# Kernel tuning notes

Measured on AMD Instinct MI355X. Metric: run time of the kernel, lower is better.

The kernel has to match this reference:

```python
import jax, jax.numpy as jnp
import numpy as np

N_NODES = 50000


def _gcn_layer(x, src, dst, W, b, n_nodes):
    # PyG GCNConv: h = x @ W, add self-loops, sym-normalized scatter-add, + bias
    h = x @ W  # [N, Dout]
    loop = jnp.arange(n_nodes, dtype=src.dtype)
    src2 = jnp.concatenate([src, loop])
    dst2 = jnp.concatenate([dst, loop])
    ones = jnp.ones(src2.shape[0], dtype=x.dtype)
    deg = jax.ops.segment_sum(ones, dst2, num_segments=n_nodes)  # in-degree w/ self-loops
    dinv = jnp.where(deg > 0, jax.lax.rsqrt(deg), 0.0)
    norm = dinv[src2] * dinv[dst2]  # [E+N]
    msg = h[src2] * norm[:, None]   # gather + scale
    out = jax.ops.segment_sum(msg, dst2, num_segments=n_nodes)  # scatter-add
    return out + b


def setup_inputs() -> dict:
    key = jax.random.key(0)
    k1, k2, k3, k4 = jax.random.split(key, 4)
    x = jax.random.normal(k1, (N_NODES, 128), dtype=jnp.float32)
    edge_index = jax.random.randint(k2, (2, 500000), 0, N_NODES, dtype=jnp.int64)
    W1 = jax.random.normal(k3, (128, 128), dtype=jnp.float32) * (1.0 / np.sqrt(128))
    b1 = jnp.zeros((128,), dtype=jnp.float32)
    W2 = jax.random.normal(k4, (128, 64), dtype=jnp.float32) * (1.0 / np.sqrt(128))
    b2 = jnp.zeros((64,), dtype=jnp.float32)
    return {"x": x, "edge_index": edge_index, "W1": W1, "b1": b1, "W2": W2, "b2": b2}


def reference(x, edge_index, W1, b1, W2, b2):
    src, dst = edge_index[0], edge_index[1]
    n = x.shape[0]
    h = _gcn_layer(x, src, dst, W1, b1, n)
    h = jax.nn.relu(h)
    out = _gcn_layer(h, src, dst, W2, b2, n)
    return out
```

## Files before the change

kernel.cpp:

```cpp
#include <hip/hip_runtime.h>
#include <hip/hip_bf16.h>
#include <cstddef>


typedef __attribute__((ext_vector_type(8))) short short8;
typedef __attribute__((ext_vector_type(4))) float f32x4;
typedef unsigned long long u64;

__device__ inline unsigned short f2bf(float f) {
    __hip_bfloat16 b = __float2bfloat16(f);
    return *reinterpret_cast<unsigned short*>(&b);
}
__device__ inline float bf2f_lo(unsigned int u) {
    unsigned int v = u << 16;
    return *reinterpret_cast<float*>(&v);
}
__device__ inline float bf2f_hi(unsigned int u) {
    unsigned int v = u & 0xffff0000u;
    return *reinterpret_cast<float*>(&v);
}
__device__ inline u64 ld_acq64(u64* p) {
    return __hip_atomic_load(p, __ATOMIC_ACQUIRE, __HIP_MEMORY_SCOPE_AGENT);
}
__device__ inline void st_rel64(u64* p, u64 v) {
    __hip_atomic_store(p, v, __ATOMIC_RELEASE, __HIP_MEMORY_SCOPE_AGENT);
}

__global__ __launch_bounds__(256) void init_kernel(int* __restrict__ deg, int N,
                                                   const float* __restrict__ W1,
                                                   const float* __restrict__ W2,
                                                   unsigned short* __restrict__ W1f,
                                                   unsigned short* __restrict__ W2f,
                                                   u64* __restrict__ lb, int ZB) {
    int b = blockIdx.x;
    int tid = threadIdx.x;
    if (b < ZB) {
        int i = (b * 256 + tid) * 4;
        if (i + 3 < N) *(int4*)(deg + i) = make_int4(0, 0, 0, 0);
        else for (; i < N; i++) deg[i] = 0;
        return;
    }
    int idx = (b - ZB) * 256 + tid;
    if (idx < 64) lb[idx] = 0;
    if (idx < 3072) {
        const float* W;
        unsigned short* Wf;
        int n, oct, Nc;
        if (idx < 2048) { W = W1; Wf = W1f; Nc = 128; n = idx >> 4; oct = idx & 15; }
        else { W = W2; Wf = W2f; Nc = 64; int i2 = idx - 2048; n = i2 >> 4; oct = i2 & 15; }
        int k0 = oct * 8;
        int ks = k0 >> 5, quad = (k0 >> 3) & 3, ntg = n >> 4;
        short8 v;
        #pragma unroll
        for (int j = 0; j < 8; j++) v[j] = (short)f2bf(W[(k0 + j) * Nc + n]);
        int off = (((ntg * 4 + ks) * 64) + (n & 15) + 16 * quad) * 8;
        *(short8*)(Wf + off) = v;
    }
}

__global__ __launch_bounds__(256) void countgemm_kernel(
    const int* __restrict__ dst, int E,
    int* __restrict__ deg, unsigned short* __restrict__ rank,
    const unsigned short* __restrict__ W1f,
    const float* __restrict__ x, unsigned short* __restrict__ h1,
    int N, int CB) {

    int b = blockIdx.x;
    int tid = threadIdx.x;

    __shared__ unsigned short As[64 * 128];

    if (b < CB) {
        int i = (b * 256 + tid) * 4;
        if (i + 3 < E) {
            int4 d = *(const int4*)(dst + i);
            unsigned short r0 = (unsigned short)atomicAdd(&deg[d.x], 1);
            unsigned short r1 = (unsigned short)atomicAdd(&deg[d.y], 1);
            unsigned short r2 = (unsigned short)atomicAdd(&deg[d.z], 1);
            unsigned short r3 = (unsigned short)atomicAdd(&deg[d.w], 1);
            *(ushort4*)(rank + i) = make_ushort4(r0, r1, r2, r3);
        } else {
            for (; i < E; i++) rank[i] = (unsigned short)atomicAdd(&deg[dst[i]], 1);
        }
        return;
    }

    constexpr int K = 128, BN = 128;
    int lane = tid & 63;
    int w = tid >> 6;
    int row0 = (b - CB) * 64;

    short8 bfr[2][4];
    #pragma unroll
    for (int nl = 0; nl < 2; nl++)
        #pragma unroll
        for (int ks = 0; ks < 4; ks++)
            bfr[nl][ks] = *(const short8*)(W1f + ((((w * 2 + nl) * 4 + ks) * 64) + lane) * 8);

    #pragma unroll
    for (int it = 0; it < 8; it++) {
        int idx = it * 256 + tid;
        int row = idx >> 5, kq = idx & 31;
        int k0 = kq * 4;
        int ks = k0 >> 5, quad = (k0 >> 3) & 3, j0 = k0 & 7, mt = row >> 4;
        ushort4 o = make_ushort4(0, 0, 0, 0);
        int gr = row0 + row;
        if (gr < N) {
            float4 a = *(const float4*)(x + (size_t)gr * K + k0);
            o.x = f2bf(a.x); o.y = f2bf(a.y); o.z = f2bf(a.z); o.w = f2bf(a.w);
        }
        int off = (((mt * 4 + ks) * 64) + (row & 15) + 16 * quad) * 8 + j0;
        *(ushort4*)(As + off) = o;
    }
    __syncthreads();

    f32x4 acc[4][2];
    #pragma unroll
    for (int mt = 0; mt < 4; mt++)
        #pragma unroll
        for (int nl = 0; nl < 2; nl++) acc[mt][nl] = (f32x4){0.f, 0.f, 0.f, 0.f};

    #pragma unroll
    for (int ks = 0; ks < 4; ks++) {
        short8 af[4];
        #pragma unroll
        for (int mt = 0; mt < 4; mt++)
            af[mt] = *(const short8*)(As + (((mt * 4 + ks) * 64) + lane) * 8);
        #pragma unroll
        for (int mt = 0; mt < 4; mt++)
            #pragma unroll
            for (int nl = 0; nl < 2; nl++)
                acc[mt][nl] = __builtin_amdgcn_mfma_f32_16x16x32_bf16(
                    af[mt], bfr[nl][ks], acc[mt][nl], 0, 0, 0);
    }

    int col16 = lane & 15;
    int rowq = lane >> 4;
    #pragma unroll
    for (int mt = 0; mt < 4; mt++) {
        #pragma unroll
        for (int nl = 0; nl < 2; nl++) {
            int gc = (w * 2 + nl) * 16 + col16;
            #pragma unroll
            for (int r = 0; r < 4; r++) {
                int lr = mt * 16 + rowq * 4 + r;
                int gr = row0 + lr;
                if (gr < N) h1[(size_t)gr * BN + gc] = f2bf(acc[mt][nl][r]);
            }
        }
    }
}

__global__ __launch_bounds__(256) void scan_lb_kernel(const int* __restrict__ deg, int N,
                                                      u64* __restrict__ lb,
                                                      int* __restrict__ offs,
                                                      float* __restrict__ dinv) {
    __shared__ int ws[4];
    __shared__ int s_prefix;
    int tid = threadIdx.x;
    int sb = blockIdx.x;
    int SB = gridDim.x;
    int lane = tid & 63;
    int wv = tid >> 6;

    int i = sb * 1024 + tid * 4;
    int v0 = (i + 0 < N) ? deg[i + 0] : 0;
    int v1 = (i + 1 < N) ? deg[i + 1] : 0;
    int v2 = (i + 2 < N) ? deg[i + 2] : 0;
    int v3 = (i + 3 < N) ? deg[i + 3] : 0;
    int tsum = v0 + v1 + v2 + v3;
    int xs = tsum;
    #pragma unroll
    for (int off = 1; off < 64; off <<= 1) {
        int y = __shfl_up(xs, off, 64);
        if (lane >= off) xs += y;
    }
    if (lane == 63) ws[wv] = xs;
    __syncthreads();
    int wprefix = 0;
    #pragma unroll
    for (int w2 = 0; w2 < 4; w2++) wprefix += (w2 < wv) ? ws[w2] : 0;
    int chunk_total = ws[0] + ws[1] + ws[2] + ws[3];

    if (wv == 0) {
        if (lane == 0)
            st_rel64(&lb[sb], ((u64)(unsigned)chunk_total << 2) | 1ull);
        int contrib = 0;
        if (sb > 0) {
            int pred = sb - 1 - lane;
            for (;;) {
                u64 v = (pred >= 0) ? ld_acq64(&lb[pred]) : 2ull;
                int flag = (int)(v & 3);
                u64 ball2 = __ballot(flag == 2);
                u64 ball0 = __ballot(flag == 0);
                if (ball2 != 0) {
                    int L = __ffsll(ball2) - 1;
                    if ((ball0 & ((1ull << L) - 1)) == 0) {
                        contrib = (lane <= L) ? (int)(unsigned)(v >> 2) : 0;
                        break;
                    }
                }
                __builtin_amdgcn_s_sleep(1);
            }
            #pragma unroll
            for (int off = 32; off >= 1; off >>= 1)
                contrib += __shfl_xor(contrib, off, 64);
        }
        if (lane == 0) {
            st_rel64(&lb[sb], ((u64)(unsigned)(contrib + chunk_total) << 2) | 2ull);
            s_prefix = contrib;
        }
    }
    __syncthreads();

    int carry = s_prefix;
    int e0 = carry + wprefix + xs - tsum;
    int e1 = e0 + v0, e2 = e1 + v1, e3 = e2 + v2;
    if (i + 0 < N) { offs[i + 0] = e0; dinv[i + 0] = rsqrtf((float)(v0 + 1)); }
    if (i + 1 < N) { offs[i + 1] = e1; dinv[i + 1] = rsqrtf((float)(v1 + 1)); }
    if (i + 2 < N) { offs[i + 2] = e2; dinv[i + 2] = rsqrtf((float)(v2 + 1)); }
    if (i + 3 < N) { offs[i + 3] = e3; dinv[i + 3] = rsqrtf((float)(v3 + 1)); }
    if (sb == SB - 1 && tid == 0) offs[N] = carry + chunk_total;
}

__global__ __launch_bounds__(256) void fill_kernel(
    const int* __restrict__ src, const int* __restrict__ dst, int E,
    const int* __restrict__ offs, const unsigned short* __restrict__ rank,
    int* __restrict__ csr) {
    int i = (blockIdx.x * 256 + threadIdx.x) * 4;
    if (i + 3 < E) {
        int4 s4 = *(const int4*)(src + i);
        int4 d4 = *(const int4*)(dst + i);
        ushort4 r4 = *(const ushort4*)(rank + i);
        csr[offs[d4.x] + (int)r4.x] = s4.x;
        csr[offs[d4.y] + (int)r4.y] = s4.y;
        csr[offs[d4.z] + (int)r4.z] = s4.z;
        csr[offs[d4.w] + (int)r4.w] = s4.w;
    } else {
        for (; i < E; i++) csr[offs[dst[i]] + (int)rank[i]] = src[i];
    }
}

__global__ __launch_bounds__(256) void aggmm_kernel(const unsigned short* __restrict__ h1,
                                                    const int* __restrict__ offs,
                                                    const int* __restrict__ csr,
                                                    const float* __restrict__ dinv,
                                                    const float* __restrict__ b1,
                                                    const unsigned short* __restrict__ W2f,
                                                    unsigned short* __restrict__ h2,
                                                    int n) {
    __shared__ unsigned short As[4 * 64 * 8];

    int tid = threadIdx.x;
    int t = tid & 63;
    int w = tid >> 6;
    int p = t >> 5;
    int t5 = t & 31;
    int nodebase = blockIdx.x * 16;
    int node0 = nodebase + w * 4;

    int ov = offs[min(node0 + min(t, 4), n)];
    int e0a[4], dega[4], nba[4], cidx[4];
    float cdw[4], dia[4];
    #pragma unroll
    for (int i = 0; i < 4; i++) {
        e0a[i] = __shfl(ov, i, 64);
        dega[i] = __shfl(ov, i + 1, 64) - e0a[i];
        nba[i] = min(dega[i], 64);
        int ce = e0a[i] + min(t, max(dega[i] - 1, 0));
        bool has = dega[i] > 0;
        cidx[i] = has ? csr[ce] : 0;
        cdw[i] = has ? dinv[cidx[i]] : 0.f;
        int node = node0 + i;
        dia[i] = (node < n) ? dinv[node] : 0.f;
    }

    short8 bw[4];
    #pragma unroll
    for (int ks = 0; ks < 4; ks++)
        bw[ks] = *(const short8*)(W2f + (((w * 4 + ks) * 64) + t) * 8);

    float4 bias = *(const float4*)(b1 + t5 * 4);

    #pragma unroll
    for (int i = 0; i < 4; i++) {
        int row16 = w * 4 + i;
        int node = node0 + i;
        float a0 = 0.f, a1 = 0.f, a2 = 0.f, a3 = 0.f;
        if (node < n) {
            if (p == 0) {
                uint2 su = *(const uint2*)(h1 + (size_t)node * 128 + t5 * 4);
                a0 = bf2f_lo(su.x) * dia[i]; a1 = bf2f_hi(su.x) * dia[i];
                a2 = bf2f_lo(su.y) * dia[i]; a3 = bf2f_hi(su.y) * dia[i];
            }
            for (int jb = 0; jb < nba[i]; jb += 8) {
                #pragma unroll
                for (int j = 0; j < 4; j++) {
                    int ee = jb + j * 2 + p;
                    int ec = min(ee, nba[i] - 1);
                    int s = __shfl(cidx[i], ec, 64);
                    float wraw = __shfl(cdw[i], ec, 64);
                    float wgt = (ee < nba[i]) ? wraw : 0.f;
                    uint2 hu = *(const uint2*)(h1 + (size_t)s * 128 + t5 * 4);
                    a0 += bf2f_lo(hu.x) * wgt; a1 += bf2f_hi(hu.x) * wgt;
                    a2 += bf2f_lo(hu.y) * wgt; a3 += bf2f_hi(hu.y) * wgt;
                }
            }
            int e1 = e0a[i] + dega[i];
            for (int eb = e0a[i] + 64; eb < e1; eb += 8) {
                #pragma unroll
                for (int j = 0; j < 4; j++) {
                    int ee = eb + j * 2 + p;
                    int ec = min(ee, e1 - 1);
                    int s = csr[ec];
                    float wgt = (ee < e1) ? dinv[s] : 0.f;
                    uint2 hu = *(const uint2*)(h1 + (size_t)s * 128 + t5 * 4);
                    a0 += bf2f_lo(hu.x) * wgt; a1 += bf2f_hi(hu.x) * wgt;
                    a2 += bf2f_lo(hu.y) * wgt; a3 += bf2f_hi(hu.y) * wgt;
                }
            }
        }
        a0 += __shfl_xor(a0, 32, 64);
        a1 += __shfl_xor(a1, 32, 64);
        a2 += __shfl_xor(a2, 32, 64);
        a3 += __shfl_xor(a3, 32, 64);
        if (p == 0) {
            if (node < n) {
                a0 = fmaxf(a0 * dia[i] + bias.x, 0.f);
                a1 = fmaxf(a1 * dia[i] + bias.y, 0.f);
                a2 = fmaxf(a2 * dia[i] + bias.z, 0.f);
                a3 = fmaxf(a3 * dia[i] + bias.w, 0.f);
            }
            int k0 = t5 * 4;
            int ks = k0 >> 5, quad = (k0 >> 3) & 3, j0 = k0 & 7;
            ushort4 pk4 = make_ushort4(f2bf(a0), f2bf(a1), f2bf(a2), f2bf(a3));
            *(ushort4*)(As + ((ks * 64) + row16 + 16 * quad) * 8 + j0) = pk4;
        }
    }
    __syncthreads();

    f32x4 acc = (f32x4){0.f, 0.f, 0.f, 0.f};
    #pragma unroll
    for (int ks = 0; ks < 4; ks++) {
        short8 af = *(const short8*)(As + ((ks * 64) + t) * 8);
        acc = __builtin_amdgcn_mfma_f32_16x16x32_bf16(af, bw[ks], acc, 0, 0, 0);
    }

    int col = w * 16 + (t & 15);
    int rowq = t >> 4;
    #pragma unroll
    for (int r = 0; r < 4; r++) {
        int gr = nodebase + rowq * 4 + r;
        if (gr < n) h2[(size_t)gr * 64 + col] = f2bf(acc[r] * dinv[gr]);
    }
}

__global__ __launch_bounds__(256) void aggout_kernel(const unsigned short* __restrict__ h2,
                                                     const int* __restrict__ offs,
                                                     const int* __restrict__ csr,
                                                     const float* __restrict__ dinv,
                                                     const float* __restrict__ b2,
                                                     float* __restrict__ out, int n) {
    int tid = threadIdx.x;
    int t = tid & 63;
    int w = tid >> 6;
    int node = blockIdx.x * 4 + w;
    if (node >= n) return;
    int p = t >> 4;
    int t4 = t & 15;

    int e0 = offs[node];
    int e1 = offs[node + 1];
    int deg = e1 - e0;
    int nb = min(deg, 64);
    int cidx = (deg > 0) ? csr[e0 + min(t, max(deg - 1, 0))] : 0;

    float a0 = 0.f, a1 = 0.f, a2 = 0.f, a3 = 0.f;
    float di = dinv[node];
    if (p == 0) {
        uint2 su = *(const uint2*)(h2 + (size_t)node * 64 + t4 * 4);
        a0 = bf2f_lo(su.x); a1 = bf2f_hi(su.x);
        a2 = bf2f_lo(su.y); a3 = bf2f_hi(su.y);
    }

    for (int jb = 0; jb < nb; jb += 8) {
        #pragma unroll
        for (int j = 0; j < 2; j++) {
            int ee = jb + j * 4 + p;
            int ec = min(ee, nb - 1);
            int s = __shfl(cidx, ec, 64);
            float wgt = (ee < deg) ? 1.f : 0.f;
            uint2 hu = *(const uint2*)(h2 + (size_t)s * 64 + t4 * 4);
            a0 += bf2f_lo(hu.x) * wgt; a1 += bf2f_hi(hu.x) * wgt;
            a2 += bf2f_lo(hu.y) * wgt; a3 += bf2f_hi(hu.y) * wgt;
        }
    }
    for (int eb = e0 + 64; eb < e1; eb += 8) {
        #pragma unroll
        for (int j = 0; j < 2; j++) {
            int ee = eb + j * 4 + p;
            int ec = min(ee, e1 - 1);
            int s = csr[ec];
            float wgt = (ee < e1) ? 1.f : 0.f;
            uint2 hu = *(const uint2*)(h2 + (size_t)s * 64 + t4 * 4);
            a0 += bf2f_lo(hu.x) * wgt; a1 += bf2f_hi(hu.x) * wgt;
            a2 += bf2f_lo(hu.y) * wgt; a3 += bf2f_hi(hu.y) * wgt;
        }
    }
    a0 += __shfl_xor(a0, 16, 64); a1 += __shfl_xor(a1, 16, 64);
    a2 += __shfl_xor(a2, 16, 64); a3 += __shfl_xor(a3, 16, 64);
    a0 += __shfl_xor(a0, 32, 64); a1 += __shfl_xor(a1, 32, 64);
    a2 += __shfl_xor(a2, 32, 64); a3 += __shfl_xor(a3, 32, 64);
    if (p == 0) {
        float4 bb = *(const float4*)(b2 + t4 * 4);
        *(float4*)(out + (size_t)node * 64 + t4 * 4) =
            make_float4(a0 * di + bb.x, a1 * di + bb.y, a2 * di + bb.z, a3 * di + bb.w);
    }
}

extern "C" void kernel_launch(void* const* d_in, const int* in_sizes, int n_in,
                              void* d_out, int out_size, void* d_ws, size_t ws_size,
                              hipStream_t stream) {
    const float* x  = (const float*)d_in[0];
    const int*   ei = (const int*)d_in[1];
    const float* W1 = (const float*)d_in[2];
    const float* b1 = (const float*)d_in[3];
    const float* W2 = (const float*)d_in[4];
    const float* b2 = (const float*)d_in[5];

    const int N = in_sizes[0] / 128;
    const int E = in_sizes[1] / 2;
    const int* src = ei;
    const int* dst = ei + E;

    char* p = (char*)d_ws;
    auto alloc = [&](size_t bytes) {
        char* r = p;
        p += (bytes + 255) & ~(size_t)255;
        return r;
    };
    int*   degi  = (int*)  alloc((size_t)N * 4);
    float* dinv  = (float*)alloc((size_t)N * 4);
    int*   offs  = (int*)  alloc((size_t)(N + 1) * 4);
    u64*   lb    = (u64*)  alloc((size_t)64 * 8);
    unsigned short* rank = (unsigned short*)alloc((size_t)E * 2);
    int*            csr  = (int*)alloc((size_t)E * 4);
    unsigned short* W1f  = (unsigned short*)alloc((size_t)128 * 128 * 2);
    unsigned short* W2f  = (unsigned short*)alloc((size_t)64 * 128 * 2);
    unsigned short* h1   = (unsigned short*)alloc((size_t)N * 128 * 2);
    unsigned short* h2   = (unsigned short*)alloc((size_t)N * 64 * 2);
    float* out = (float*)d_out;

    const int GB = (N + 63) / 64;
    const int SB = (N + 1023) / 1024;
    const int CB = (E / 4 + 255) / 256;
    const int ZB = (N + 1023) / 1024;
    const int FB4 = (E / 4 + 255) / 256;

    init_kernel<<<ZB + 12, 256, 0, stream>>>(degi, N, W1, W2, W1f, W2f, lb, ZB);
    countgemm_kernel<<<CB + GB, 256, 0, stream>>>(dst, E, degi, rank, W1f,
                                                  x, h1, N, CB);
    scan_lb_kernel<<<SB, 256, 0, stream>>>(degi, N, lb, offs, dinv);
    fill_kernel<<<FB4, 256, 0, stream>>>(src, dst, E, offs, rank, csr);
    aggmm_kernel<<<(N + 15) / 16, 256, 0, stream>>>(h1, offs, csr, dinv, b1, W2f, h2, N);
    aggout_kernel<<<(N + 3) / 4, 256, 0, stream>>>(h2, offs, csr, dinv, b2, out, N);
}
```

Before: 173.1 us.

## Fuse all GCN stages into one persistent cooperative kernel with grid syncs

Replaces the six separate kernel launches (init, count+GEMM, scan, CSR fill, layer-1 aggregate+matmul, layer-2 aggregate) with a single cooperative persistent kernel. Stages are separated by grid.sync() and each stage uses grid-stride loops over its original work units. The scan now runs on the first SB blocks while the remaining blocks do the x@W1 GEMM, instead of fusing GEMM with degree counting. This removes per-launch overhead and inter-kernel gaps. In exchange it adds grid-wide barriers and caps the grid at a fixed number of resident blocks, and launch_bounds(256,4) may constrain registers in the heavier phases.

Measured after the change: 521.7 us. +201.4%, slower.

```diff
diff --git a/kernel.cpp b/kernel.cpp
--- a/kernel.cpp
+++ b/kernel.cpp
@@ -1,6 +1,9 @@
 #include <hip/hip_runtime.h>
 #include <hip/hip_bf16.h>
+#include <hip/hip_cooperative_groups.h>
 #include <cstddef>
+
+namespace cg = cooperative_groups;
 
 
 typedef __attribute__((ext_vector_type(8))) short short8;
@@ -26,52 +29,51 @@
     __hip_atomic_store(p, v, __ATOMIC_RELEASE, __HIP_MEMORY_SCOPE_AGENT);
 }
 
-__global__ __launch_bounds__(256) void init_kernel(int* __restrict__ deg, int N,
-                                                   const float* __restrict__ W1,
-                                                   const float* __restrict__ W2,
-                                                   unsigned short* __restrict__ W1f,
-                                                   unsigned short* __restrict__ W2f,
-                                                   u64* __restrict__ lb, int ZB) {
+__global__ __launch_bounds__(256, 4) void fused_kernel(
+    const int* __restrict__ src, const int* __restrict__ dst, int E,
+    int* __restrict__ deg, unsigned short* __restrict__ rank,
+    const float* __restrict__ W1, const float* __restrict__ W2,
+    unsigned short* __restrict__ W1f, unsigned short* __restrict__ W2f,
+    u64* __restrict__ lb,
+    const float* __restrict__ x, unsigned short* __restrict__ h1,
+    int* __restrict__ offs, float* __restrict__ dinv,
+    int* __restrict__ csr,
+    const float* __restrict__ b1, const float* __restrict__ b2,
+    unsigned short* __restrict__ h2, float* __restrict__ out,
+    int N, int CB, int SB, int GB, int AT, int OT) {
+
+    cg::grid_group grid = cg::this_grid();
     int b = blockIdx.x;
+    int NB = gridDim.x;
     int tid = threadIdx.x;
-    if (b < ZB) {
-        int i = (b * 256 + tid) * 4;
-        if (i + 3 < N) *(int4*)(deg + i) = make_int4(0, 0, 0, 0);
-        else for (; i < N; i++) deg[i] = 0;
-        return;
-    }
-    int idx = (b - ZB) * 256 + tid;
-    if (idx < 64) lb[idx] = 0;
-    if (idx < 3072) {
-        const float* W;
-        unsigned short* Wf;
-        int n, oct, Nc;
-        if (idx < 2048) { W = W1; Wf = W1f; Nc = 128; n = idx >> 4; oct = idx & 15; }
-        else { W = W2; Wf = W2f; Nc = 64; int i2 = idx - 2048; n = i2 >> 4; oct = i2 & 15; }
-        int k0 = oct * 8;
-        int ks = k0 >> 5, quad = (k0 >> 3) & 3, ntg = n >> 4;
-        short8 v;
-        #pragma unroll
-        for (int j = 0; j < 8; j++) v[j] = (short)f2bf(W[(k0 + j) * Nc + n]);
-        int off = (((ntg * 4 + ks) * 64) + (n & 15) + 16 * quad) * 8;
-        *(short8*)(Wf + off) = v;
-    }
-}
-
-__global__ __launch_bounds__(256) void countgemm_kernel(
-    const int* __restrict__ dst, int E,
-    int* __restrict__ deg, unsigned short* __restrict__ rank,
-    const unsigned short* __restrict__ W1f,
-    const float* __restrict__ x, unsigned short* __restrict__ h1,
-    int N, int CB) {
-
-    int b = blockIdx.x;
-    int tid = threadIdx.x;
 
     __shared__ unsigned short As[64 * 128];
-
-    if (b < CB) {
-        int i = (b * 256 + tid) * 4;
+    __shared__ int ws[4];
+    __shared__ int s_prefix;
+
+    {
+        for (int gi = b * 256 + tid; gi < N; gi += NB * 256) deg[gi] = 0;
+        int gi = b * 256 + tid;
+        if (gi < 64) lb[gi] = 0;
+        if (gi < 3072) {
+            const float* W;
+            unsigned short* Wf;
+            int n, oct, Nc;
+            if (gi < 2048) { W = W1; Wf = W1f; Nc = 128; n = gi >> 4; oct = gi & 15; }
+            else { W = W2; Wf = W2f; Nc = 64; int i2 = gi - 2048; n = i2 >> 4; oct = i2 & 15; }
+            int k0 = oct * 8;
+            int ks = k0 >> 5, quad = (k0 >> 3) & 3, ntg = n >> 4;
+            short8 v;
+            #pragma unroll
+            for (int j = 0; j < 8; j++) v[j] = (short)f2bf(W[(k0 + j) * Nc + n]);
+            int off = (((ntg * 4 + ks) * 64) + (n & 15) + 16 * quad) * 8;
+            *(short8*)(Wf + off) = v;
+        }
+    }
+    grid.sync();
+
+    for (int u = b; u < CB; u += NB) {
+        int i = (u * 256 + tid) * 4;
         if (i + 3 < E) {
             int4 d = *(const int4*)(dst + i);
             unsigned short r0 = (unsigned short)atomicAdd(&deg[d.x], 1);
@@ -82,339 +84,323 @@
         } else {
             for (; i < E; i++) rank[i] = (unsigned short)atomicAdd(&deg[dst[i]], 1);
         }
-        return;
-    }
-
-    constexpr int K = 128, BN = 128;
-    int lane = tid & 63;
-    int w = tid >> 6;
-    int row0 = (b - CB) * 64;
-
-    short8 bfr[2][4];
-    #pragma unroll
-    for (int nl = 0; nl < 2; nl++)
+    }
+    grid.sync();
+
+    if (b < SB) {
+        int sb = b;
+        int lane = tid & 63;
+        int wv = tid >> 6;
+        int i = sb * 1024 + tid * 4;
+        int v0 = (i + 0 < N) ? deg[i + 0] : 0;
+        int v1 = (i + 1 < N) ? deg[i + 1] : 0;
+        int v2 = (i + 2 < N) ? deg[i + 2] : 0;
+        int v3 = (i + 3 < N) ? deg[i + 3] : 0;
+        int tsum = v0 + v1 + v2 + v3;
+        int xs = tsum;
         #pragma unroll
-        for (int ks = 0; ks < 4; ks++)
-            bfr[nl][ks] = *(const short8*)(W1f + ((((w * 2 + nl) * 4 + ks) * 64) + lane) * 8);
-
-    #pragma unroll
-    for (int it = 0; it < 8; it++) {
-        int idx = it * 256 + tid;
-        int row = idx >> 5, kq = idx & 31;
-        int k0 = kq * 4;
-        int ks = k0 >> 5, quad = (k0 >> 3) & 3, j0 = k0 & 7, mt = row >> 4;
-        ushort4 o = make_ushort4(0, 0, 0, 0);
-        int gr = row0 + row;
-        if (gr < N) {
-            float4 a = *(const float4*)(x + (size_t)gr * K + k0);
-            o.x = f2bf(a.x); o.y = f2bf(a.y); o.z = f2bf(a.z); o.w = f2bf(a.w);
-        }
-        int off = (((mt * 4 + ks) * 64) + (row & 15) + 16 * quad) * 8 + j0;
-        *(ushort4*)(As + off) = o;
-    }
-    __syncthreads();
-
-    f32x4 acc[4][2];
-    #pragma unroll
-    for (int mt = 0; mt < 4; mt++)
+        for (int off = 1; off < 64; off <<= 1) {
+            int y = __shfl_up(xs, off, 64);
+            if (lane >= off) xs += y;
+        }
+        if (lane == 63) ws[wv] = xs;
+        __syncthreads();
+        int wprefix = 0;
         #pragma unroll
-        for (int nl = 0; nl < 2; nl++) acc[mt][nl] = (f32x4){0.f, 0.f, 0.f, 0.f};
-
-    #pragma unroll
-    for (int ks = 0; ks < 4; ks++) {
-        short8 af[4];
-        #pragma unroll
-        for (int mt = 0; mt < 4; mt++)
-            af[mt] = *(const short8*)(As + (((mt * 4 + ks) * 64) + lane) * 8);
-        #pragma unroll
-        for (int mt = 0; mt < 4; mt++)
+        for (int w2 = 0; w2 < 4; w2++) wprefix += (w2 < wv) ? ws[w2] : 0;
+        int chunk_total = ws[0] + ws[1] + ws[2] + ws[3];
+
+        if (wv == 0) {
+            if (lane == 0)
+                st_rel64(&lb[sb], ((u64)(unsigned)chunk_total << 2) | 1ull);
+            int contrib = 0;
+            if (sb > 0) {
+                int pred = sb - 1 - lane;
+                for (;;) {
+                    u64 v = (pred >= 0) ? ld_acq64(&lb[pred]) : 2ull;
+                    int flag = (int)(v & 3);
+                    u64 ball2 = __ballot(flag == 2);
+                    u64 ball0 = __ballot(flag == 0);
+                    if (ball2 != 0) {
+                        int L = __ffsll(ball2) - 1;
+                        if ((ball0 & ((1ull << L) - 1)) == 0) {
+                            contrib = (lane <= L) ? (int)(unsigned)(v >> 2) : 0;
+                            break;
+                        }
+                    }
+                    __builtin_amdgcn_s_sleep(1);
+                }
+                #pragma unroll
+                for (int off = 32; off >= 1; off >>= 1)
+                    contrib += __shfl_xor(contrib, off, 64);
+            }
+            if (lane == 0) {
+                st_rel64(&lb[sb], ((u64)(unsigned)(contrib + chunk_total) << 2) | 2ull);
+                s_prefix = contrib;
+            }
+        }
+        __syncthreads();
+
+        int carry = s_prefix;
+        int e0 = carry + wprefix + xs - tsum;
+        int e1 = e0 + v0, e2 = e1 + v1, e3 = e2 + v2;
+        if (i + 0 < N) { offs[i + 0] = e0; dinv[i + 0] = rsqrtf((float)(v0 + 1)); }
+        if (i + 1 < N) { offs[i + 1] = e1; dinv[i + 1] = rsqrtf((float)(v1 + 1)); }
+        if (i + 2 < N) { offs[i + 2] = e2; dinv[i + 2] = rsqrtf((float)(v2 + 1)); }
+        if (i + 3 < N) { offs[i + 3] = e3; dinv[i + 3] = rsqrtf((float)(v3 + 1)); }
+        if (sb == SB - 1 && tid == 0) offs[N] = carry + chunk_total;
+    } else {
+        constexpr int K = 128, BN = 128;
+        int lane = tid & 63;
+        int w = tid >> 6;
+        for (int g = b - SB; g < GB; g += NB - SB) {
+            int row0 = g * 64;
+            short8 bfr[2][4];
             #pragma unroll
             for (int nl = 0; nl < 2; nl++)
-                acc[mt][nl] = __builtin_amdgcn_mfma_f32_16x16x32_bf16(
-                    af[mt], bfr[nl][ks], acc[mt][nl], 0, 0, 0);
-    }
-
-    int col16 = lane & 15;
-    int rowq = lane >> 4;
-    #pragma unroll
-    for (int mt = 0; mt < 4; mt++) {
-        #pragma unroll
-        for (int nl = 0; nl < 2; nl++) {
-            int gc = (w * 2 + nl) * 16 + col16;
+                #pragma unroll
+                for (int ks = 0; ks < 4; ks++)
+                    bfr[nl][ks] = *(const short8*)(W1f + ((((w * 2 + nl) * 4 + ks) * 64) + lane) * 8);
+
+            #pragma unroll
+            for (int it = 0; it < 8; it++) {
+                int idx = it * 256 + tid;
+                int row = idx >> 5, kq = idx & 31;
+                int k0 = kq * 4;
+                int ks = k0 >> 5, quad = (k0 >> 3) & 3, j0 = k0 & 7, mt = row >> 4;
+                ushort4 o = make_ushort4(0, 0, 0, 0);
+                int gr = row0 + row;
+                if (gr < N) {
+                    float4 a = *(const float4*)(x + (size_t)gr * K + k0);
+                    o.x = f2bf(a.x); o.y = f2bf(a.y); o.z = f2bf(a.z); o.w = f2bf(a.w);
+                }
+                int off = (((mt * 4 + ks) * 64) + (row & 15) + 16 * quad) * 8 + j0;
+                *(ushort4*)(As + off) = o;
+            }
+            __syncthreads();
+
+            f32x4 acc[4][2];
+            #pragma unroll
+            for (int mt = 0; mt < 4; mt++)
+                #pragma unroll
+                for (int nl = 0; nl < 2; nl++) acc[mt][nl] = (f32x4){0.f, 0.f, 0.f, 0.f};
+
+            #pragma unroll
+            for (int ks = 0; ks < 4; ks++) {
+                short8 af[4];
+                #pragma unroll
+                for (int mt = 0; mt < 4; mt++)
+                    af[mt] = *(const short8*)(As + (((mt * 4 + ks) * 64) + lane) * 8);
+                #pragma unroll
+                for (int mt = 0; mt < 4; mt++)
+                    #pragma unroll
+                    for (int nl = 0; nl < 2; nl++)
+                        acc[mt][nl] = __builtin_amdgcn_mfma_f32_16x16x32_bf16(
+                            af[mt], bfr[nl][ks], acc[mt][nl], 0, 0, 0);
+            }
+
+            int col16 = lane & 15;
+            int rowq = lane >> 4;
+            #pragma unroll
+            for (int mt = 0; mt < 4; mt++) {
+                #pragma unroll
+                for (int nl = 0; nl < 2; nl++) {
+                    int gc = (w * 2 + nl) * 16 + col16;
+                    #pragma unroll
+                    for (int r = 0; r < 4; r++) {
+                        int lr = mt * 16 + rowq * 4 + r;
+                        int gr = row0 + lr;
+                        if (gr < N) h1[(size_t)gr * BN + gc] = f2bf(acc[mt][nl][r]);
+                    }
+                }
+            }
+            __syncthreads();
+        }
+    }
+    grid.sync();
+
+    for (int u = b; u < CB; u += NB) {
+        int i = (u * 256 + tid) * 4;
+        if (i + 3 < E) {
+            int4 s4 = *(const int4*)(src + i);
+            int4 d4 = *(const int4*)(dst + i);
+            ushort4 r4 = *(const ushort4*)(rank + i);
+            csr[offs[d4.x] + (int)r4.x] = s4.x;
+            csr[offs[d4.y] + (int)r4.y] = s4.y;
+            csr[offs[d4.z] + (int)r4.z] = s4.z;
+            csr[offs[d4.w] + (int)r4.w] = s4.w;
+        } else {
+            for (; i < E; i++) csr[offs[dst[i]] + (int)rank[i]] = src[i];
+        }
+    }
+    grid.sync();
+
+    {
+        int t = tid & 63;
+        int w = tid >> 6;
+        int p = t >> 5;
+        int t5 = t & 31;
+        for (int g = b; g < AT; g += NB) {
+            int nodebase = g * 16;
+            int node0 = nodebase + w * 4;
+
+            int ov = offs[min(node0 + min(t, 4), N)];
+            int e0a[4], dega[4], nba[4], cidx[4];
+            float cdw[4], dia[4];
+            #pragma unroll
+            for (int i = 0; i < 4; i++) {
+                e0a[i] = __shfl(ov, i, 64);
+                dega[i] = __shfl(ov, i + 1, 64) - e0a[i];
+                nba[i] = min(dega[i], 64);
+                int ce = e0a[i] + min(t, max(dega[i] - 1, 0));
+                bool has = dega[i] > 0;
+                cidx[i] = has ? csr[ce] : 0;
+                cdw[i] = has ? dinv[cidx[i]] : 0.f;
+                int node = node0 + i;
+                dia[i] = (node < N) ? dinv[node] : 0.f;
+            }
+
+            short8 bw[4];
+            #pragma unroll
+            for (int ks = 0; ks < 4; ks++)
+                bw[ks] = *(const short8*)(W2f + (((w * 4 + ks) * 64) + t) * 8);
+
+            float4 bias = *(const float4*)(b1 + t5 * 4);
+
+            #pragma unroll
+            for (int i = 0; i < 4; i++) {
+                int row16 = w * 4 + i;
+                int node = node0 + i;
+                float a0 = 0.f, a1 = 0.f, a2 = 0.f, a3 = 0.f;
+                if (node < N) {
+                    if (p == 0) {
+                        uint2 su = *(const uint2*)(h1 + (size_t)node * 128 + t5 * 4);
+                        a0 = bf2f_lo(su.x) * dia[i]; a1 = bf2f_hi(su.x) * dia[i];
+                        a2 = bf2f_lo(su.y) * dia[i]; a3 = bf2f_hi(su.y) * dia[i];
+                    }
+                    for (int jb = 0; jb < nba[i]; jb += 8) {
+                        #pragma unroll
+                        for (int j = 0; j < 4; j++) {
+                            int ee = jb + j * 2 + p;
+                            int ec = min(ee, nba[i] - 1);
+                            int s = __shfl(cidx[i], ec, 64);
+                            float wraw = __shfl(cdw[i], ec, 64);
+                            float wgt = (ee < nba[i]) ? wraw : 0.f;
+                            uint2 hu = *(const uint2*)(h1 + (size_t)s * 128 + t5 * 4);
+                            a0 += bf2f_lo(hu.x) * wgt; a1 += bf2f_hi(hu.x) * wgt;
+                            a2 += bf2f_lo(hu.y) * wgt; a3 += bf2f_hi(hu.y) * wgt;
+                        }
+                    }
+                    int e1 = e0a[i] + dega[i];
+                    for (int eb = e0a[i] + 64; eb < e1; eb += 8) {
+                        #pragma unroll
+                        for (int j = 0; j < 4; j++) {
+                            int ee = eb + j * 2 + p;
+                            int ec = min(ee, e1 - 1);
+                            int s = csr[ec];
+                            float wgt = (ee < e1) ? dinv[s] : 0.f;
+                            uint2 hu = *(const uint2*)(h1 + (size_t)s * 128 + t5 * 4);
+                            a0 += bf2f_lo(hu.x) * wgt; a1 += bf2f_hi(hu.x) * wgt;
+                            a2 += bf2f_lo(hu.y) * wgt; a3 += bf2f_hi(hu.y) * wgt;
+                        }
+                    }
+                }
+                a0 += __shfl_xor(a0, 32, 64);
+                a1 += __shfl_xor(a1, 32, 64);
+                a2 += __shfl_xor(a2, 32, 64);
+                a3 += __shfl_xor(a3, 32, 64);
+                if (p == 0) {
+                    if (node < N) {
+                        a0 = fmaxf(a0 * dia[i] + bias.x, 0.f);
+                        a1 = fmaxf(a1 * dia[i] + bias.y, 0.f);
+                        a2 = fmaxf(a2 * dia[i] + bias.z, 0.f);
+                        a3 = fmaxf(a3 * dia[i] + bias.w, 0.f);
+                    }
+                    int k0 = t5 * 4;
+                    int ks = k0 >> 5, quad = (k0 >> 3) & 3, j0 = k0 & 7;
+                    ushort4 pk4 = make_ushort4(f2bf(a0), f2bf(a1), f2bf(a2), f2bf(a3));
+                    *(ushort4*)(As + ((ks * 64) + row16 + 16 * quad) * 8 + j0) = pk4;
+                }
+            }
+            __syncthreads();
+
+            f32x4 acc = (f32x4){0.f, 0.f, 0.f, 0.f};
+            #pragma unroll
+            for (int ks = 0; ks < 4; ks++) {
+                short8 af = *(const short8*)(As + ((ks * 64) + t) * 8);
+                acc = __builtin_amdgcn_mfma_f32_16x16x32_bf16(af, bw[ks], acc, 0, 0, 0);
+            }
+
+            int col = w * 16 + (t & 15);
+            int rowq = t >> 4;
             #pragma unroll
             for (int r = 0; r < 4; r++) {
-                int lr = mt * 16 + rowq * 4 + r;
-                int gr = row0 + lr;
-                if (gr < N) h1[(size_t)gr * BN + gc] = f2bf(acc[mt][nl][r]);
-            }
-        }
-    }
-}
-
-__global__ __launch_bounds__(256) void scan_lb_kernel(const int* __restrict__ deg, int N,
-                                                      u64* __restrict__ lb,
-                                                      int* __restrict__ offs,
-                                                      float* __restrict__ dinv) {
-    __shared__ int ws[4];
-    __shared__ int s_prefix;
-    int tid = threadIdx.x;
-    int sb = blockIdx.x;
-    int SB = gridDim.x;
-    int lane = tid & 63;
-    int wv = tid >> 6;
-
-    int i = sb * 1024 + tid * 4;
-    int v0 = (i + 0 < N) ? deg[i + 0] : 0;
-    int v1 = (i + 1 < N) ? deg[i + 1] : 0;
-    int v2 = (i + 2 < N) ? deg[i + 2] : 0;
-    int v3 = (i + 3 < N) ? deg[i + 3] : 0;
-    int tsum = v0 + v1 + v2 + v3;
-    int xs = tsum;
-    #pragma unroll
-    for (int off = 1; off < 64; off <<= 1) {
-        int y = __shfl_up(xs, off, 64);
-        if (lane >= off) xs += y;
-    }
-    if (lane == 63) ws[wv] = xs;
-    __syncthreads();
-    int wprefix = 0;
-    #pragma unroll
-    for (int w2 = 0; w2 < 4; w2++) wprefix += (w2 < wv) ? ws[w2] : 0;
-    int chunk_total = ws[0] + ws[1] + ws[2] + ws[3];
-
-    if (wv == 0) {
-        if (lane == 0)
-            st_rel64(&lb[sb], ((u64)(unsigned)chunk_total << 2) | 1ull);
-        int contrib = 0;
-        if (sb > 0) {
-            int pred = sb - 1 - lane;
-            for (;;) {
-                u64 v = (pred >= 0) ? ld_acq64(&lb[pred]) : 2ull;
-                int flag = (int)(v & 3);
-                u64 ball2 = __ballot(flag == 2);
-                u64 ball0 = __ballot(flag == 0);
-                if (ball2 != 0) {
-                    int L = __ffsll(ball2) - 1;
-                    if ((ball0 & ((1ull << L) - 1)) == 0) {
-                        contrib = (lane <= L) ? (int)(unsigned)(v >> 2) : 0;
-                        break;
-                    }
-                }
-                __builtin_amdgcn_s_sleep(1);
-            }
-            #pragma unroll
-            for (int off = 32; off >= 1; off >>= 1)
-                contrib += __shfl_xor(contrib, off, 64);
-        }
-        if (lane == 0) {
-            st_rel64(&lb[sb], ((u64)(unsigned)(contrib + chunk_total) << 2) | 2ull);
-            s_prefix = contrib;
-        }
-    }
-    __syncthreads();
-
-    int carry = s_prefix;
-    int e0 = carry + wprefix + xs - tsum;
-    int e1 = e0 + v0, e2 = e1 + v1, e3 = e2 + v2;
-    if (i + 0 < N) { offs[i + 0] = e0; dinv[i + 0] = rsqrtf((float)(v0 + 1)); }
-    if (i + 1 < N) { offs[i + 1] = e1; dinv[i + 1] = rsqrtf((float)(v1 + 1)); }
-    if (i + 2 < N) { offs[i + 2] = e2; dinv[i + 2] = rsqrtf((float)(v2 + 1)); }
-    if (i + 3 < N) { offs[i + 3] = e3; dinv[i + 3] = rsqrtf((float)(v3 + 1)); }
-    if (sb == SB - 1 && tid == 0) offs[N] = carry + chunk_total;
-}
-
-__global__ __launch_bounds__(256) void fill_kernel(
-    const int* __restrict__ src, const int* __restrict__ dst, int E,
-    const int* __restrict__ offs, const unsigned short* __restrict__ rank,
-    int* __restrict__ csr) {
-    int i = (blockIdx.x * 256 + threadIdx.x) * 4;
-    if (i + 3 < E) {
-        int4 s4 = *(const int4*)(src + i);
-        int4 d4 = *(const int4*)(dst + i);
-        ushort4 r4 = *(const ushort4*)(rank + i);
-        csr[offs[d4.x] + (int)r4.x] = s4.x;
-        csr[offs[d4.y] + (int)r4.y] = s4.y;
-        csr[offs[d4.z] + (int)r4.z] = s4.z;
-        csr[offs[d4.w] + (int)r4.w] = s4.w;
-    } else {
-        for (; i < E; i++) csr[offs[dst[i]] + (int)rank[i]] = src[i];
-    }
-}
-
-__global__ __launch_bounds__(256) void aggmm_kernel(const unsigned short* __restrict__ h1,
-                                                    const int* __restrict__ offs,
-                                                    const int* __restrict__ csr,
-                                                    const float* __restrict__ dinv,
-                                                    const float* __restrict__ b1,
-                                                    const unsigned short* __restrict__ W2f,
-                                                    unsigned short* __restrict__ h2,
-                                                    int n) {
-    __shared__ unsigned short As[4 * 64 * 8];
-
-    int tid = threadIdx.x;
-    int t = tid & 63;
-    int w = tid >> 6;
-    int p = t >> 5;
-    int t5 = t & 31;
-    int nodebase = blockIdx.x * 16;
-    int node0 = nodebase + w * 4;
-
-    int ov = offs[min(node0 + min(t, 4), n)];
-    int e0a[4], dega[4], nba[4], cidx[4];
-    float cdw[4], dia[4];
-    #pragma unroll
-    for (int i = 0; i < 4; i++) {
-        e0a[i] = __shfl(ov, i, 64);
-        dega[i] = __shfl(ov, i + 1, 64) - e0a[i];
-        nba[i] = min(dega[i], 64);
-        int ce = e0a[i] + min(t, max(dega[i] - 1, 0));
-        bool has = dega[i] > 0;
-        cidx[i] = has ? csr[ce] : 0;
-        cdw[i] = has ? dinv[cidx[i]] : 0.f;
-        int node = node0 + i;
-        dia[i] = (node < n) ? dinv[node] : 0.f;
-    }
-
-    short8 bw[4];
-    #pragma unroll
-    for (int ks = 0; ks < 4; ks++)
-        bw[ks] = *(const short8*)(W2f + (((w * 4 + ks) * 64) + t) * 8);
-
-    float4 bias = *(const float4*)(b1 + t5 * 4);
-
-    #pragma unroll
-    for (int i = 0; i < 4; i++) {
-        int row16 = w * 4 + i;
-        int node = node0 + i;
-        float a0 = 0.f, a1 = 0.f, a2 = 0.f, a3 = 0.f;
-        if (node < n) {
-            if (p == 0) {
-                uint2 su = *(const uint2*)(h1 + (size_t)node * 128 + t5 * 4);
-                a0 = bf2f_lo(su.x) * dia[i]; a1 = bf2f_hi(su.x) * dia[i];
-                a2 = bf2f_lo(su.y) * dia[i]; a3 = bf2f_hi(su.y) * dia[i];
-            }
-            for (int jb = 0; jb < nba[i]; jb += 8) {
-                #pragma unroll
-                for (int j = 0; j < 4; j++) {
-                    int ee = jb + j * 2 + p;
-                    int ec = min(ee, nba[i] - 1);
-                    int s = __shfl(cidx[i], ec, 64);
-                    float wraw = __shfl(cdw[i], ec, 64);
-                    float wgt = (ee < nba[i]) ? wraw : 0.f;
-                    uint2 hu = *(const uint2*)(h1 + (size_t)s * 128 + t5 * 4);
-                    a0 += bf2f_lo(hu.x) * wgt; a1 += bf2f_hi(hu.x) * wgt;
-                    a2 += bf2f_lo(hu.y) * wgt; a3 += bf2f_hi(hu.y) * wgt;
-                }
-            }
-            int e1 = e0a[i] + dega[i];
-            for (int eb = e0a[i] + 64; eb < e1; eb += 8) {
-                #pragma unroll
-                for (int j = 0; j < 4; j++) {
-                    int ee = eb + j * 2 + p;
-                    int ec = min(ee, e1 - 1);
-                    int s = csr[ec];
-                    float wgt = (ee < e1) ? dinv[s] : 0.f;
-                    uint2 hu = *(const uint2*)(h1 + (size_t)s * 128 + t5 * 4);
-                    a0 += bf2f_lo(hu.x) * wgt; a1 += bf2f_hi(hu.x) * wgt;
-                    a2 += bf2f_lo(hu.y) * wgt; a3 += bf2f_hi(hu.y) * wgt;
-                }
-            }
-        }
-        a0 += __shfl_xor(a0, 32, 64);
-        a1 += __shfl_xor(a1, 32, 64);
-        a2 += __shfl_xor(a2, 32, 64);
-        a3 += __shfl_xor(a3, 32, 64);
-        if (p == 0) {
-            if (node < n) {
-                a0 = fmaxf(a0 * dia[i] + bias.x, 0.f);
-                a1 = fmaxf(a1 * dia[i] + bias.y, 0.f);
-                a2 = fmaxf(a2 * dia[i] + bias.z, 0.f);
-                a3 = fmaxf(a3 * dia[i] + bias.w, 0.f);
-            }
-            int k0 = t5 * 4;
-            int ks = k0 >> 5, quad = (k0 >> 3) & 3, j0 = k0 & 7;
-            ushort4 pk4 = make_ushort4(f2bf(a0), f2bf(a1), f2bf(a2), f2bf(a3));
-            *(ushort4*)(As + ((ks * 64) + row16 + 16 * quad) * 8 + j0) = pk4;
-        }
-    }
-    __syncthreads();
-
-    f32x4 acc = (f32x4){0.f, 0.f, 0.f, 0.f};
-    #pragma unroll
-    for (int ks = 0; ks < 4; ks++) {
-        short8 af = *(const short8*)(As + ((ks * 64) + t) * 8);
-        acc = __builtin_amdgcn_mfma_f32_16x16x32_bf16(af, bw[ks], acc, 0, 0, 0);
-    }
-
-    int col = w * 16 + (t & 15);
-    int rowq = t >> 4;
-    #pragma unroll
-    for (int r = 0; r < 4; r++) {
-        int gr = nodebase + rowq * 4 + r;
-        if (gr < n) h2[(size_t)gr * 64 + col] = f2bf(acc[r] * dinv[gr]);
-    }
-}
-
-__global__ __launch_bounds__(256) void aggout_kernel(const unsigned short* __restrict__ h2,
-                                                     const int* __restrict__ offs,
-                                                     const int* __restrict__ csr,
-                                                     const float* __restrict__ dinv,
-                                                     const float* __restrict__ b2,
-                                                     float* __restrict__ out, int n) {
-    int tid = threadIdx.x;
-    int t = tid & 63;
-    int w = tid >> 6;
-    int node = blockIdx.x * 4 + w;
-    if (node >= n) return;
-    int p = t >> 4;
-    int t4 = t & 15;
-
-    int e0 = offs[node];
-    int e1 = offs[node + 1];
-    int deg = e1 - e0;
-    int nb = min(deg, 64);
-    int cidx = (deg > 0) ? csr[e0 + min(t, max(deg - 1, 0))] : 0;
-
-    float a0 = 0.f, a1 = 0.f, a2 = 0.f, a3 = 0.f;
-    float di = dinv[node];
-    if (p == 0) {
-        uint2 su = *(const uint2*)(h2 + (size_t)node * 64 + t4 * 4);
-        a0 = bf2f_lo(su.x); a1 = bf2f_hi(su.x);
-        a2 = bf2f_lo(su.y); a3 = bf2f_hi(su.y);
-    }
-
-    for (int jb = 0; jb < nb; jb += 8) {
-        #pragma unroll
-        for (int j = 0; j < 2; j++) {
-            int ee = jb + j * 4 + p;
-            int ec = min(ee, nb - 1);
-            int s = __shfl(cidx, ec, 64);
-            float wgt = (ee < deg) ? 1.f : 0.f;
-            uint2 hu = *(const uint2*)(h2 + (size_t)s * 64 + t4 * 4);
-            a0 += bf2f_lo(hu.x) * wgt; a1 += bf2f_hi(hu.x) * wgt;
-            a2 += bf2f_lo(hu.y) * wgt; a3 += bf2f_hi(hu.y) * wgt;
-        }
-    }
-    for (int eb = e0 + 64; eb < e1; eb += 8) {
-        #pragma unroll
-        for (int j = 0; j < 2; j++) {
-            int ee = eb + j * 4 + p;
-            int ec = min(ee, e1 - 1);
-            int s = csr[ec];
-            float wgt = (ee < e1) ? 1.f : 0.f;
-            uint2 hu = *(const uint2*)(h2 + (size_t)s * 64 + t4 * 4);
-            a0 += bf2f_lo(hu.x) * wgt; a1 += bf2f_hi(hu.x) * wgt;
-            a2 += bf2f_lo(hu.y) * wgt; a3 += bf2f_hi(hu.y) * wgt;
-        }
-    }
-    a0 += __shfl_xor(a0, 16, 64); a1 += __shfl_xor(a1, 16, 64);
-    a2 += __shfl_xor(a2, 16, 64); a3 += __shfl_xor(a3, 16, 64);
-    a0 += __shfl_xor(a0, 32, 64); a1 += __shfl_xor(a1, 32, 64);
-    a2 += __shfl_xor(a2, 32, 64); a3 += __shfl_xor(a3, 32, 64);
-    if (p == 0) {
-        float4 bb = *(const float4*)(b2 + t4 * 4);
-        *(float4*)(out + (size_t)node * 64 + t4 * 4) =
-            make_float4(a0 * di + bb.x, a1 * di + bb.y, a2 * di + bb.z, a3 * di + bb.w);
+                int gr = nodebase + rowq * 4 + r;
+                if (gr < N) h2[(size_t)gr * 64 + col] = f2bf(acc[r] * dinv[gr]);
+            }
+            __syncthreads();
+        }
+    }
+    grid.sync();
+
+    {
+        int t = tid & 63;
+        int w = tid >> 6;
+        int p = t >> 4;
+        int t4 = t & 15;
+        for (int g = b; g < OT; g += NB) {
+            int node = g * 4 + w;
+            if (node < N) {
+                int e0 = offs[node];
+                int e1 = offs[node + 1];
+                int dg = e1 - e0;
+                int nb = min(dg, 64);
+                int cidx = (dg > 0) ? csr[e0 + min(t, max(dg - 1, 0))] : 0;
+
+                float a0 = 0.f, a1 = 0.f, a2 = 0.f, a3 = 0.f;
+                float di = dinv[node];
+                if (p == 0) {
+                    uint2 su = *(const uint2*)(h2 + (size_t)node * 64 + t4 * 4);
+                    a0 = bf2f_lo(su.x); a1 = bf2f_hi(su.x);
+                    a2 = bf2f_lo(su.y); a3 = bf2f_hi(su.y);
+                }
+
+                for (int jb = 0; jb < nb; jb += 8) {
+                    #pragma unroll
+                    for (int j = 0; j < 2; j++) {
+                        int ee = jb + j * 4 + p;
+                        int ec = min(ee, nb - 1);
+                        int s = __shfl(cidx, ec, 64);
+                        float wgt = (ee < dg) ? 1.f : 0.f;
+                        uint2 hu = *(const uint2*)(h2 + (size_t)s * 64 + t4 * 4);
+                        a0 += bf2f_lo(hu.x) * wgt; a1 += bf2f_hi(hu.x) * wgt;
+                        a2 += bf2f_lo(hu.y) * wgt; a3 += bf2f_hi(hu.y) * wgt;
+                    }
+                }
+                for (int eb = e0 + 64; eb < e1; eb += 8) {
+                    #pragma unroll
+                    for (int j = 0; j < 2; j++) {
+                        int ee = eb + j * 4 + p;
+                        int ec = min(ee, e1 - 1);
+                        int s = csr[ec];
+                        float wgt = (ee < e1) ? 1.f : 0.f;
+                        uint2 hu = *(const uint2*)(h2 + (size_t)s * 64 + t4 * 4);
+                        a0 += bf2f_lo(hu.x) * wgt; a1 += bf2f_hi(hu.x) * wgt;
+                        a2 += bf2f_lo(hu.y) * wgt; a3 += bf2f_hi(hu.y) * wgt;
+                    }
+                }
+                a0 += __shfl_xor(a0, 16, 64); a1 += __shfl_xor(a1, 16, 64);
+                a2 += __shfl_xor(a2, 16, 64); a3 += __shfl_xor(a3, 16, 64);
+                a0 += __shfl_xor(a0, 32, 64); a1 += __shfl_xor(a1, 32, 64);
+                a2 += __shfl_xor(a2, 32, 64); a3 += __shfl_xor(a3, 32, 64);
+                if (p == 0) {
+                    float4 bb = *(const float4*)(b2 + t4 * 4);
+                    *(float4*)(out + (size_t)node * 64 + t4 * 4) =
+                        make_float4(a0 * di + bb.x, a1 * di + bb.y,
+                                    a2 * di + bb.z, a3 * di + bb.w);
+                }
+            }
+        }
     }
 }
 
@@ -428,8 +414,8 @@
     const float* W2 = (const float*)d_in[4];
     const float* b2 = (const float*)d_in[5];
 
-    const int N = in_sizes[0] / 128;
-    const int E = in_sizes[1] / 2;
+    int N = in_sizes[0] / 128;
+    int E = in_sizes[1] / 2;
     const int* src = ei;
     const int* dst = ei + E;
 
@@ -451,17 +437,30 @@
     unsigned short* h2   = (unsigned short*)alloc((size_t)N * 64 * 2);
     float* out = (float*)d_out;
 
-    const int GB = (N + 63) / 64;
-    const int SB = (N + 1023) / 1024;
-    const int CB = (E / 4 + 255) / 256;
-    const int ZB = (N + 1023) / 1024;
-    const int FB4 = (E / 4 + 255) / 256;
-
-    init_kernel<<<ZB + 12, 256, 0, stream>>>(degi, N, W1, W2, W1f, W2f, lb, ZB);
-    countgemm_kernel<<<CB + GB, 256, 0, stream>>>(dst, E, degi, rank, W1f,
-                                                  x, h1, N, CB);
-    scan_lb_kernel<<<SB, 256, 0, stream>>>(degi, N, lb, offs, dinv);
-    fill_kernel<<<FB4, 256, 0, stream>>>(src, dst, E, offs, rank, csr);
-    aggmm_kernel<<<(N + 15) / 16, 256, 0, stream>>>(h1, offs, csr, dinv, b1, W2f, h2, N);
-    aggout_kernel<<<(N + 3) / 4, 256, 0, stream>>>(h2, offs, csr, dinv, b2, out, N);
-}
+    int CB = (E / 4 + 255) / 256;
+    int SB = (N + 1023) / 1024;
+    int GB = (N + 63) / 64;
+    int AT = (N + 15) / 16;
+    int OT = (N + 3) / 4;
+
+    int maxActive = 0;
+    hipOccupancyMaxActiveBlocksPerMultiprocessor(&maxActive, fused_kernel, 256, 0);
+    if (maxActive < 1) maxActive = 1;
+    int NB = maxActive * 256;
+    if (NB > 2048) NB = 2048;
+
+    void* args[] = { (void*)&src, (void*)&dst, (void*)&E,
+                     (void*)&degi, (void*)&rank,
+                     (void*)&W1, (void*)&W2, (void*)&W1f, (void*)&W2f,
+                     (void*)&lb,
+                     (void*)&x, (void*)&h1,
+                     (void*)&offs, (void*)&dinv,
+                     (void*)&csr,
+                     (void*)&b1, (void*)&b2,
+                     (void*)&h2, (void*)&out,
+                     (void*)&N, (void*)&CB, (void*)&SB, (void*)&GB,
+                     (void*)&AT, (void*)&OT };
+
+    hipLaunchCooperativeKernel((void*)fused_kernel, dim3(NB), dim3(256),
+                               args, 0, stream);
+}
```
